# Performance work log

Measured on AMD Instinct MI355X. Metric: run time of the kernel, lower is better.

The kernel has to match this reference:

```python
import jax, jax.numpy as jnp
import numpy as np

N_HEAD = 8
D_HEAD = 128   # dim_k = dim_q = dim_v
SEG_LEN = 512
EPS = 1e-6


def setup_inputs() -> dict:
    key = jax.random.key(0)
    ks = jax.random.split(key, 8)
    B, T, D = 2, 4096, 1024
    scale = 0.02
    x = jax.random.normal(ks[0], (B, T, D), dtype=jnp.float32)
    w_q = jax.random.normal(ks[1], (D, N_HEAD * D_HEAD), dtype=jnp.float32) * scale
    w_k = jax.random.normal(ks[2], (D, N_HEAD * D_HEAD), dtype=jnp.float32) * scale
    w_v = jax.random.normal(ks[3], (D, N_HEAD * D_HEAD), dtype=jnp.float32) * scale
    b_q = jnp.zeros((N_HEAD * D_HEAD,), jnp.float32)
    b_k = jnp.zeros((N_HEAD * D_HEAD,), jnp.float32)
    b_v = jnp.zeros((N_HEAD * D_HEAD,), jnp.float32)
    beta = jnp.zeros((N_HEAD,), jnp.float32)
    return {"x": x, "w_q": w_q, "b_q": b_q, "w_k": w_k, "b_k": b_k,
            "w_v": w_v, "b_v": b_v, "beta": beta}


def _heads(y, B, T):
    # [B,T,H*D] -> [B,H,T,D]
    return y.reshape(B, T, N_HEAD, D_HEAD).transpose(0, 2, 1, 3)


def reference(x, w_q, b_q, w_k, b_k, w_v, b_v, beta):
    B, T, _ = x.shape
    S = T // SEG_LEN
    q = _heads(x @ w_q + b_q, B, T)
    k = _heads(x @ w_k + b_k, B, T)
    v = _heads(x @ w_v + b_v, B, T)

    # segment: [B,H,T,D] -> [S,B,H,L,D]
    def seg(y):
        return y.reshape(B, N_HEAD, S, SEG_LEN, D_HEAD).transpose(2, 0, 1, 3, 4)
    qs, ks_, vs = seg(q), seg(k), seg(v)

    causal = jnp.tril(jnp.ones((SEG_LEN, SEG_LEN), bool))
    gate = jax.nn.sigmoid(beta).reshape(1, N_HEAD, 1, 1)
    inv_sqrt_d = 1.0 / jnp.sqrt(jnp.asarray(D_HEAD, x.dtype))

    def step(carry, segdat):
        M, z = carry                      # M: [B,H,Dk,Dv], z: [B,H,Dk]
        qc, kc, vc = segdat               # [B,H,L,D]
        sq = jax.nn.elu(qc) + 1.0
        sk = jax.nn.elu(kc) + 1.0
        # retrieval from memory BEFORE update
        a_mem = jnp.einsum('bhld,bhde->bhle', sq, M) / (
            jnp.einsum('bhld,bhd->bhl', sq, z)[..., None] + EPS)
        # delta-rule memory update
        retr_k = jnp.einsum('bhld,bhde->bhle', sk, M) / (
            jnp.einsum('bhld,bhd->bhl', sk, z)[..., None] + EPS)
        M = M + jnp.einsum('bhld,bhle->bhde', sk, vc - retr_k)
        z = z + sk.sum(axis=2)
        # local causal dot-product attention within the segment
        scores = jnp.einsum('bhld,bhmd->bhlm', qc, kc) * inv_sqrt_d
        scores = jnp.where(causal, scores, jnp.asarray(-1e30, scores.dtype))
        a_dot = jnp.einsum('bhlm,bhmd->bhld', jax.nn.softmax(scores, axis=-1), vc)
        # long-term context injection
        a = gate * a_mem + (1.0 - gate) * a_dot
        return (M, z), a

    M0 = jnp.zeros((B, N_HEAD, D_HEAD, D_HEAD), x.dtype)
    z0 = jnp.zeros((B, N_HEAD, D_HEAD), x.dtype)
    _, out = jax.lax.scan(step, (M0, z0), (qs, ks_, vs))
    # [S,B,H,L,D] -> [B,T,H*D]
    out = out.transpose(1, 3, 0, 2, 4).reshape(B, T, N_HEAD * D_HEAD)
    # wait: axes of out are [S,B,H,L,D]; reorder to [B,S,L,H,D]
    return out


# fix ordering: define reference properly (overrides above draft path)
def reference(x, w_q, b_q, w_k, b_k, w_v, b_v, beta):
    B, T, _ = x.shape
    S = T // SEG_LEN
    q = _heads(x @ w_q + b_q, B, T)
    k = _heads(x @ w_k + b_k, B, T)
    v = _heads(x @ w_v + b_v, B, T)

    def seg(y):
        return y.reshape(B, N_HEAD, S, SEG_LEN, D_HEAD).transpose(2, 0, 1, 3, 4)
    qs, ks_, vs = seg(q), seg(k), seg(v)

    causal = jnp.tril(jnp.ones((SEG_LEN, SEG_LEN), bool))
    gate = jax.nn.sigmoid(beta).reshape(1, N_HEAD, 1, 1)
    inv_sqrt_d = 1.0 / jnp.sqrt(jnp.asarray(D_HEAD, x.dtype))

    def step(carry, segdat):
        M, z = carry
        qc, kc, vc = segdat
        sq = jax.nn.elu(qc) + 1.0
        sk = jax.nn.elu(kc) + 1.0
        a_mem = jnp.einsum('bhld,bhde->bhle', sq, M) / (
            jnp.einsum('bhld,bhd->bhl', sq, z)[..., None] + EPS)
        retr_k = jnp.einsum('bhld,bhde->bhle', sk, M) / (
            jnp.einsum('bhld,bhd->bhl', sk, z)[..., None] + EPS)
        M = M + jnp.einsum('bhld,bhle->bhde', sk, vc - retr_k)
        z = z + sk.sum(axis=2)
        scores = jnp.einsum('bhld,bhmd->bhlm', qc, kc) * inv_sqrt_d
        scores = jnp.where(causal, scores, jnp.asarray(-1e30, scores.dtype))
        a_dot = jnp.einsum('bhlm,bhmd->bhld', jax.nn.softmax(scores, axis=-1), vc)
        a = gate * a_mem + (1.0 - gate) * a_dot
        return (M, z), a

    M0 = jnp.zeros((B, N_HEAD, D_HEAD, D_HEAD), x.dtype)
    z0 = jnp.zeros((B, N_HEAD, D_HEAD), x.dtype)
    _, out = jax.lax.scan(step, (M0, z0), (qs, ks_, vs))  # [S,B,H,L,D]
    out = out.transpose(1, 0, 3, 2, 4).reshape(B, T, N_HEAD * D_HEAD)
    return out
```

## Files before the change

### kernel.cpp

```cpp
#include <hip/hip_runtime.h>
#include <hip/hip_bf16.h>

typedef __attribute__((ext_vector_type(8))) short bf16x8;
typedef __attribute__((ext_vector_type(4))) float f32x4;
typedef unsigned short u16;
typedef unsigned int u32;

#define DEV static __device__ __forceinline__

DEV float bf2f(u16 u){ u32 x = ((u32)u)<<16; float f; __builtin_memcpy(&f,&x,4); return f; }
DEV u16 f2bf(float f){ u32 x; __builtin_memcpy(&x,&f,4); return (u16)((x + 0x7fffu + ((x>>16)&1u))>>16); }
DEV float elu1(float x){ return x > 0.f ? x + 1.f : __expf(x); }

DEV void gload16(const u16* g, u16* l){
  __builtin_amdgcn_global_load_lds(
      (const __attribute__((address_space(1))) unsigned int*)(g),
      (__attribute__((address_space(3))) unsigned int*)(l), 16, 0, 0);
}

#define MFMA(a,b,c) __builtin_amdgcn_mfma_f32_16x16x32_bf16((a),(b),(c),0,0,0)

#define NB 2
#define NT 4096
#define NH 8
#define DH 128
#define NS 8
#define SL 512
#define ND 1024
#define N3 3072
#define EPS 1e-6f

__global__ __launch_bounds__(256) void k_xc(const float* __restrict__ x, u16* __restrict__ xb){
  int i = blockIdx.x*256 + threadIdx.x;
  const float4 v0 = *(const float4*)(x + (size_t)i*8);
  const float4 v1 = *(const float4*)(x + (size_t)i*8 + 4);
  bf16x8 o;
  o[0]=(short)f2bf(v0.x); o[1]=(short)f2bf(v0.y); o[2]=(short)f2bf(v0.z); o[3]=(short)f2bf(v0.w);
  o[4]=(short)f2bf(v1.x); o[5]=(short)f2bf(v1.y); o[6]=(short)f2bf(v1.z); o[7]=(short)f2bf(v1.w);
  *(bf16x8*)(xb + (size_t)i*8) = o;
}

__global__ __launch_bounds__(256) void k_wt(const float* __restrict__ wq,
                                            const float* __restrict__ wk,
                                            const float* __restrict__ wv,
                                            u16* __restrict__ wt,
                                            float* __restrict__ cs){
  __shared__ float t[32][33];
  const int z = blockIdx.z;
  const float* w = (z==0) ? wq : (z==1 ? wk : wv);
  const int k0 = blockIdx.x*32, n0 = blockIdx.y*32;
  const int tx = threadIdx.x, ty = threadIdx.y;
  if (z==0 && blockIdx.x==0 && blockIdx.y==0){
    const int tid = ty*32 + tx;
#pragma unroll
    for (int i=0;i<64;i++) cs[tid + i*256] = 0.f;
  }
#pragma unroll
  for (int i=0;i<4;i++) t[ty+i*8][tx] = w[(size_t)(k0+ty+i*8)*ND + n0+tx];
  __syncthreads();
#pragma unroll
  for (int i=0;i<4;i++)
    wt[(size_t)(z*ND + n0+ty+i*8)*ND + k0+tx] = f2bf(t[tx][ty+i*8]);
}

__global__ __launch_bounds__(256) void k_gemm(const u16* __restrict__ xb,
                                              const u16* __restrict__ wt,
                                              const float* __restrict__ bq,
                                              const float* __restrict__ bk,
                                              const float* __restrict__ bv,
                                              u16* __restrict__ qkv){
  __shared__ __align__(16) u16 As[128*64];
  __shared__ __align__(16) u16 Bs[128*64];
  const int m0 = blockIdx.x*128, n0 = blockIdx.y*128;
  const int tid = threadIdx.x;
  const int w = tid>>6, lane = tid&63, g = lane>>4, li = lane&15;
  const int wr = w>>1, wc = w&1;
  const int srow = lane>>3;
  const int ssl  = (lane&7) ^ srow;
  f32x4 z4 = {0.f,0.f,0.f,0.f};
  f32x4 acc[4][4];
#pragma unroll
  for (int mi=0;mi<4;mi++)
#pragma unroll
    for (int ni=0;ni<4;ni++) acc[mi][ni] = z4;

  for (int kt=0; kt<16; ++kt){
    const int k0 = kt*64;
#pragma unroll
    for (int i=0;i<4;i++){
      const int c = i*4 + w;
      const int row = c*8 + srow;
      gload16(xb + (size_t)(m0+row)*ND + k0 + ssl*8, As + c*512);
      gload16(wt + (size_t)(n0+row)*ND + k0 + ssl*8, Bs + c*512);
    }
    __syncthreads();
#pragma unroll
    for (int kk=0;kk<2;kk++){
      bf16x8 a[4], bb[4];
#pragma unroll
      for (int mi=0;mi<4;mi++){
        int row = wr*64 + mi*16 + li;
        int slot = kk*4 + g;
        a[mi] = *(const bf16x8*)(As + row*64 + ((slot^(row&7))<<3));
      }
#pragma unroll
      for (int ni=0;ni<4;ni++){
        int row = wc*64 + ni*16 + li;
        int slot = kk*4 + g;
        bb[ni] = *(const bf16x8*)(Bs + row*64 + ((slot^(row&7))<<3));
      }
#pragma unroll
      for (int mi=0;mi<4;mi++)
#pragma unroll
        for (int ni=0;ni<4;ni++)
          acc[mi][ni] = MFMA(a[mi], bb[ni], acc[mi][ni]);
    }
    __syncthreads();
  }
#pragma unroll
  for (int ni=0;ni<4;ni++){
    int n = n0 + wc*64 + ni*16 + li;
    float bias = (n < ND) ? bq[n] : (n < 2*ND ? bk[n-ND] : bv[n-2*ND]);
#pragma unroll
    for (int mi=0;mi<4;mi++)
#pragma unroll
      for (int rr=0;rr<4;rr++){
        int m = m0 + wr*64 + mi*16 + 4*g + rr;
        qkv[(size_t)m*N3 + n] = f2bf(acc[mi][ni][rr] + bias);
      }
  }
}

__global__ __launch_bounds__(256) void k_tr(const u16* __restrict__ qkv,
                                            u16* __restrict__ vt,
                                            u16* __restrict__ pkT,
                                            float* __restrict__ cs){
  __shared__ __align__(4) u16 t[64*66];
  __shared__ float pf[8][64];
  const int t0 = blockIdx.x*64, d0 = blockIdx.y*64;
  const int z = blockIdx.z, bh = z>>1, part = z&1;
  const int b = bh>>3, h = bh&7;
  const int basec = (part ? 2*ND : ND) + h*DH;
  const int tid = threadIdx.x;
  float s0 = 0.f, s1 = 0.f;
#pragma unroll
  for (int i=0;i<8;i++){
    int fp = tid + i*256;
    int row = fp>>5, c2 = (fp&31)*2;
    ushort2 v = *(const ushort2*)(qkv + (size_t)(b*NT + t0+row)*N3 + basec + d0 + c2);
    if (!part){
      float e0 = elu1(bf2f(v.x)), e1 = elu1(bf2f(v.y));
      s0 += e0; s1 += e1;
      v.x = f2bf(e0); v.y = f2bf(e1);
    }
    *(ushort2*)(t + row*66 + c2) = v;
  }
  if (!part){ pf[tid>>5][(tid&31)*2] = s0; pf[tid>>5][(tid&31)*2+1] = s1; }
  __syncthreads();
  u16* dst = part ? vt : pkT;
#pragma unroll
  for (int i=0;i<8;i++){
    int fp = tid + i*256;
    int dr = fp>>5, c2 = (fp&31)*2;
    ushort2 v; v.x = t[c2*66 + dr]; v.y = t[(c2+1)*66 + dr];
    *(ushort2*)(dst + (size_t)(bh*DH + d0+dr)*NT + t0 + c2) = v;
  }
  if (!part && tid < 64){
    float a = 0.f;
#pragma unroll
    for (int r=0;r<8;r++) a += pf[r][tid];
    const int bhs = b*64 + h*8 + (t0>>9);
    atomicAdd(&cs[(size_t)bhs*DH + d0 + tid], a);
  }
}

__global__ __launch_bounds__(512) void k_dinv(const u16* __restrict__ qkv,
                                              const float* __restrict__ cs,
                                              float* __restrict__ dinvK){
  const int bhs = blockIdx.x, half = blockIdx.y;
  const int b = bhs>>6, h = (bhs>>3)&7, s = bhs&7;
  const int tid = threadIdx.x, w = tid>>6, lane = tid&63, grp = lane>>4, li = lane&15;
  __shared__ float zl[128];
  if (tid < 128){
    float a = 0.f;
    for (int sp=0; sp<s; ++sp) a += cs[(size_t)(bhs - s + sp)*DH + tid];
    zl[tid] = a;
  }
  __syncthreads();
#pragma unroll
  for (int it=0; it<8; ++it){
    const int r = half*256 + w*32 + it*4 + grp;
    bf16x8 v = *(const bf16x8*)(qkv + (size_t)(b*NT + s*SL + r)*N3 + ND + h*DH + li*8);
    float p = 0.f;
#pragma unroll
    for (int j=0;j<8;j++) p += elu1(bf2f((u16)v[j])) * zl[li*8+j];
    p += __shfl_xor(p,1); p += __shfl_xor(p,2);
    p += __shfl_xor(p,4); p += __shfl_xor(p,8);
    if (li == 0) dinvK[(size_t)bhs*SL + r] = 1.f/(p + EPS);
  }
}

__global__ __launch_bounds__(512) void k_gram(const u16* __restrict__ pkT,
                                              const u16* __restrict__ vtb,
                                              const float* __restrict__ dinvK,
                                              u16* __restrict__ G, float* __restrict__ Bm){
  const int bhs = blockIdx.x, ec = blockIdx.y;
  const int bh = bhs>>3, s = bhs&7, tb = s*SL;
  const int tid = threadIdx.x, w = tid>>6, lane = tid&63, g = lane>>4, li = lane&15;
  __shared__ __align__(16) u16 Bk[32*512];
  __shared__ __align__(16) u16 Bv[32*512];
  __shared__ float dv[512];
  dv[tid] = dinvK[(size_t)bhs*SL + tid];
#pragma unroll
  for (int i=0;i<4;i++){
    const int ee = i*8 + w;
    const size_t rowo = ((size_t)bh*DH + ec*32 + ee)*NT + tb + ((lane^w)<<3);
    gload16(pkT + rowo, Bk + ee*512);
    gload16(vtb + rowo, Bv + ee*512);
  }
  __syncthreads();
  f32x4 z4 = {0.f,0.f,0.f,0.f};
  f32x4 Ga[2] = {z4,z4}, Ba[2] = {z4,z4};
  const u16* arow = pkT + ((size_t)bh*DH + 16*w + li)*NT + tb;
  for (int ks=0; ks<16; ++ks){
    const int r0 = ks*32 + g*8;
    bf16x8 araw = *(const bf16x8*)(arow + r0);
    float4 d0 = *(const float4*)(dv + r0);
    float4 d1 = *(const float4*)(dv + r0 + 4);
    bf16x8 ascl;
    ascl[0] = (short)f2bf(bf2f((u16)araw[0]) * d0.x);
    ascl[1] = (short)f2bf(bf2f((u16)araw[1]) * d0.y);
    ascl[2] = (short)f2bf(bf2f((u16)araw[2]) * d0.z);
    ascl[3] = (short)f2bf(bf2f((u16)araw[3]) * d0.w);
    ascl[4] = (short)f2bf(bf2f((u16)araw[4]) * d1.x);
    ascl[5] = (short)f2bf(bf2f((u16)araw[5]) * d1.y);
    ascl[6] = (short)f2bf(bf2f((u16)araw[6]) * d1.z);
    ascl[7] = (short)f2bf(bf2f((u16)araw[7]) * d1.w);
    const int slot = ks*4 + g;
#pragma unroll
    for (int ni=0;ni<2;ni++){
      const int ee = ni*16 + li;
      bf16x8 bk8 = *(const bf16x8*)(Bk + ee*512 + ((slot^(li&7))<<3));
      bf16x8 bv8 = *(const bf16x8*)(Bv + ee*512 + ((slot^(li&7))<<3));
      Ga[ni] = MFMA(ascl, bk8, Ga[ni]);
      Ba[ni] = MFMA(araw, bv8, Ba[ni]);
    }
  }
#pragma unroll
  for (int ni=0;ni<2;ni++)
#pragma unroll
    for (int rr=0;rr<4;rr++){
      const int dd = 16*w + 4*g + rr;
      const int ee = ec*32 + ni*16 + li;
      G[((size_t)bhs*DH + dd)*DH + ee] = f2bf(Ga[ni][rr]);
      Bm[((size_t)bhs*DH + dd)*DH + ee] = Ba[ni][rr];
    }
}

__global__ __launch_bounds__(512) void k_scan(const u16* __restrict__ G,
                                              const float* __restrict__ Bm,
                                              u16* __restrict__ MTs){
  const int bh = blockIdx.x;
  const int tid = threadIdx.x, w = tid>>6, lane = tid&63, g = lane>>4, li = lane&15;
  __shared__ __align__(16) u16 MT[16384];
  for (int i = tid; i < 16384; i += 512) MT[i] = 0;
  __syncthreads();
  for (int s=0;s<NS;s++){
    const size_t bhs = (size_t)bh*NS + s;
    for (int f = tid; f < 2048; f += 512){
      int e = f>>4, sl = f&15;
      bf16x8 v = *(const bf16x8*)(MT + e*128 + ((sl^(e&7))<<3));
      *(bf16x8*)(MTs + bhs*16384 + e*128 + sl*8) = v;
    }
    __syncthreads();
    f32x4 z4 = {0.f,0.f,0.f,0.f};
    f32x4 acc[8];
#pragma unroll
    for (int i=0;i<8;i++) acc[i] = z4;
#pragma unroll
    for (int ks=0;ks<4;ks++){
      bf16x8 a = *(const bf16x8*)(G + (bhs*DH + 16*w + li)*DH + ks*32 + g*8);
#pragma unroll
      for (int ni=0;ni<8;ni++){
        int e = ni*16 + li;
        int sl = ks*4 + g;
        bf16x8 bfr = *(const bf16x8*)(MT + e*128 + ((sl^(e&7))<<3));
        acc[ni] = MFMA(a, bfr, acc[ni]);
      }
    }
    __syncthreads();
#pragma unroll
    for (int ni=0;ni<8;ni++)
#pragma unroll
      for (int rr=0;rr<4;rr++){
        int dd = 16*w + 4*g + rr, ee = ni*16 + li;
        float delta = Bm[(bhs*DH + dd)*DH + ee] - acc[ni][rr];
        int idx = ee*128 + (((dd>>3)^(ee&7))<<3) + (dd&7);
        MT[idx] = f2bf(bf2f(MT[idx]) + delta);
      }
    __syncthreads();
  }
}

__global__ __launch_bounds__(512) void k_attn(const u16* __restrict__ qkv,
                                              const u16* __restrict__ vtb,
                                              const u16* __restrict__ MTs,
                                              const float* __restrict__ cs,
                                              const float* __restrict__ beta,
                                              float* __restrict__ out){
  const int bhs = blockIdx.x, half = blockIdx.y;
  const int b = bhs>>6, h = (bhs>>3)&7, s = bhs&7, bh = bhs>>3;
  const int tid = threadIdx.x, w = tid>>6, lane = tid&63, g = lane>>4, li = lane&15;
  const int jq = (w < 4) ? (half + 2*w) : (15 - half - 2*(w-4));
  const int qb = jq*32;
  const float gate = 1.f/(1.f + __expf(-beta[h]));
  const float isd = 0.08838834764831845f;
  const float L2E = 1.4426950408889634f;
  __shared__ __align__(16) u16 P[8*1024];
  __shared__ float zl[128];
  __shared__ float dinvW[8][32];
  u16* Pw = P + w*1024;

  if (tid < 128){
    float a = 0.f;
    for (int sp=0; sp<s; ++sp) a += cs[(size_t)(bhs - s + sp)*DH + tid];
    zl[tid] = a;
  }
  __syncthreads();

  {
    const int r = qb + (lane&31);
    const int dh = (lane>>5)*64;
    const u16* qrow = qkv + (size_t)(b*NT + s*SL + r)*N3 + h*DH + dh;
    float p = 0.f;
#pragma unroll
    for (int j=0;j<64;j+=8){
      bf16x8 v = *(const bf16x8*)(qrow + j);
#pragma unroll
      for (int t=0;t<8;t++) p += elu1(bf2f((u16)v[t])) * zl[dh + j + t];
    }
    p += __shfl_xor(p, 32);
    if (lane < 32) dinvW[w][lane] = 1.f/(p + EPS);
  }

  bf16x8 qf[2][4];
#pragma unroll
  for (int mf=0; mf<2; ++mf)
#pragma unroll
    for (int kf=0; kf<4; ++kf)
      qf[mf][kf] = *(const bf16x8*)(qkv + (size_t)(b*NT + s*SL + qb + mf*16 + li)*N3 + h*DH + kf*32 + g*8);

  f32x4 z4 = {0.f,0.f,0.f,0.f};
  f32x4 O[2][8];
  float lr[2][4];
#pragma unroll
  for (int mf=0;mf<2;++mf){
#pragma unroll
    for (int nf=0;nf<8;++nf) O[mf][nf] = z4;
#pragma unroll
    for (int rr=0;rr<4;++rr) lr[mf][rr] = 0.f;
  }

  const int nch = jq + 1;
  for (int c=0; c<nch; ++c){
    const int kb = c*32;
    f32x4 sa[2][2];
#pragma unroll
    for (int mf=0;mf<2;++mf)
#pragma unroll
      for (int nf=0;nf<2;++nf) sa[mf][nf] = z4;
#pragma unroll
    for (int kf=0; kf<4; ++kf)
#pragma unroll
      for (int nf=0; nf<2; ++nf){
        bf16x8 bk8 = *(const bf16x8*)(qkv + (size_t)(b*NT + s*SL + kb + nf*16 + li)*N3 + ND + h*DH + kf*32 + g*8);
        sa[0][nf] = MFMA(qf[0][kf], bk8, sa[0][nf]);
        sa[1][nf] = MFMA(qf[1][kf], bk8, sa[1][nf]);
      }
    float pv[2][2][4];
#pragma unroll
    for (int mf=0;mf<2;++mf)
#pragma unroll
      for (int rr=0;rr<4;++rr){
        int row = qb + mf*16 + 4*g + rr;
        float rs = 0.f;
#pragma unroll
        for (int nf=0;nf<2;++nf){
          int col = kb + nf*16 + li;
          float sc = sa[mf][nf][rr]*isd;
          float p = (col > row) ? 0.f : exp2f(sc*L2E);
          pv[mf][nf][rr] = p; rs += p;
        }
        rs += __shfl_xor(rs, 1); rs += __shfl_xor(rs, 2);
        rs += __shfl_xor(rs, 4); rs += __shfl_xor(rs, 8);
        lr[mf][rr] += rs;
      }
#pragma unroll
    for (int mf=0;mf<2;++mf)
#pragma unroll
      for (int nf=0;nf<2;++nf)
#pragma unroll
        for (int rr=0;rr<4;++rr){
          int row = mf*16 + 4*g + rr, col = nf*16 + li;
          Pw[row*32 + (((col>>3)^(row&3))<<3) + (col&7)] = f2bf(pv[mf][nf][rr]);
        }
    bf16x8 pa[2];
#pragma unroll
    for (int mf=0;mf<2;++mf){
      int row = mf*16 + li;
      pa[mf] = *(const bf16x8*)(Pw + row*32 + ((g^(row&3))<<3));
    }
#pragma unroll
    for (int nf=0;nf<8;++nf){
      bf16x8 bv8 = *(const bf16x8*)(vtb + ((size_t)bh*DH + nf*16 + li)*NT + s*SL + kb + g*8);
      O[0][nf] = MFMA(pa[0], bv8, O[0][nf]);
      O[1][nf] = MFMA(pa[1], bv8, O[1][nf]);
    }
  }

  f32x4 Am[2][8];
#pragma unroll
  for (int mf=0;mf<2;++mf)
#pragma unroll
    for (int nf=0;nf<8;++nf) Am[mf][nf] = z4;
#pragma unroll
  for (int ks=0;ks<4;++ks){
    bf16x8 pq[2];
#pragma unroll
    for (int mf=0;mf<2;++mf){
      bf16x8 raw = qf[mf][ks];
#pragma unroll
      for (int j=0;j<8;j++) raw[j] = (short)f2bf(elu1(bf2f((u16)raw[j])));
      pq[mf] = raw;
    }
#pragma unroll
    for (int nf=0;nf<8;++nf){
      bf16x8 bfr = *(const bf16x8*)(MTs + ((size_t)bhs*DH + nf*16 + li)*DH + ks*32 + g*8);
      Am[0][nf] = MFMA(pq[0], bfr, Am[0][nf]);
      Am[1][nf] = MFMA(pq[1], bfr, Am[1][nf]);
    }
  }

  const float og = 1.f - gate;
#pragma unroll
  for (int mf=0;mf<2;++mf)
#pragma unroll
    for (int rr=0;rr<4;++rr){
      int row = qb + mf*16 + 4*g + rr;
      float invd = og / lr[mf][rr];
      float dv = gate * dinvW[w][row - qb];
#pragma unroll
      for (int nf=0;nf<8;++nf)
        out[(size_t)(b*NT + s*SL + row)*ND + h*DH + nf*16 + li] =
            O[mf][nf][rr]*invd + Am[mf][nf][rr]*dv;
    }
}

extern "C" void kernel_launch(void* const* d_in, const int* in_sizes, int n_in,
                              void* d_out, int out_size, void* d_ws, size_t ws_size,
                              hipStream_t stream) {
  (void)in_sizes; (void)n_in; (void)out_size; (void)ws_size;
  const float* x    = (const float*)d_in[0];
  const float* wq   = (const float*)d_in[1];
  const float* bq   = (const float*)d_in[2];
  const float* wk   = (const float*)d_in[3];
  const float* bk   = (const float*)d_in[4];
  const float* wv   = (const float*)d_in[5];
  const float* bv   = (const float*)d_in[6];
  const float* beta = (const float*)d_in[7];
  float* out = (float*)d_out;
  char* ws = (char*)d_ws;

  u16*   wt  = (u16*)  (ws + 0);
  u16*   qkv = (u16*)  (ws + 6291456);
  u16*   vt  = (u16*)  (ws + 56623104);
  u16*   pkT = (u16*)  (ws + 73400320);
  u16*   G   = (u16*)  (ws + 90177536);
  float* Bm  = (float*)(ws + 94371840);
  u16*   MTs = (u16*)  (ws + 102760448);
  float* cs  = (float*)(ws + 106954752);
  u16*   xb  = vt;
  float* dinvK = (float*)(ws + 107020288);

  hipLaunchKernelGGL(k_xc,    dim3(4096),    dim3(256),  0, stream, x, xb);
  hipLaunchKernelGGL(k_wt,    dim3(32,32,3), dim3(32,8), 0, stream, wq, wk, wv, wt, cs);
  hipLaunchKernelGGL(k_gemm,  dim3(64,24),   dim3(256),  0, stream, xb, wt, bq, bk, bv, qkv);
  hipLaunchKernelGGL(k_tr,    dim3(64,2,32), dim3(256),  0, stream, qkv, vt, pkT, cs);
  hipLaunchKernelGGL(k_dinv,  dim3(128,2),   dim3(512),  0, stream, qkv, cs, dinvK);
  hipLaunchKernelGGL(k_gram,  dim3(128,4),   dim3(512),  0, stream, pkT, vt, dinvK, G, Bm);
  hipLaunchKernelGGL(k_scan,  dim3(16),      dim3(512),  0, stream, G, Bm, MTs);
  hipLaunchKernelGGL(k_attn,  dim3(128,2),   dim3(512),  0, stream, qkv, vt, MTs, cs, beta, out);
}
```

Baseline: 201.6 us.

## Split memory scan across column blocks and stage GEMM epilogue through LDS

```diff
diff --git a/kernel.cpp b/kernel.cpp
--- a/kernel.cpp
+++ b/kernel.cpp
@@ -117,17 +117,28 @@
     }
     __syncthreads();
   }
+
+  u16* SC = (w < 2 ? As : Bs) + (w&1)*4096;
 #pragma unroll
   for (int ni=0;ni<4;ni++){
-    int n = n0 + wc*64 + ni*16 + li;
-    float bias = (n < ND) ? bq[n] : (n < 2*ND ? bk[n-ND] : bv[n-2*ND]);
+    const int n = n0 + wc*64 + ni*16 + li;
+    const float bias = (n < ND) ? bq[n] : (n < 2*ND ? bk[n-ND] : bv[n-2*ND]);
 #pragma unroll
     for (int mi=0;mi<4;mi++)
 #pragma unroll
       for (int rr=0;rr<4;rr++){
-        int m = m0 + wr*64 + mi*16 + 4*g + rr;
-        qkv[(size_t)m*N3 + n] = f2bf(acc[mi][ni][rr] + bias);
+        const int ml = mi*16 + 4*g + rr;
+        const int nl = ni*16 + li;
+        SC[ml*64 + (((nl>>3)^(ml&7))<<3) + (nl&7)] = f2bf(acc[mi][ni][rr] + bias);
       }
+  }
+  __syncthreads();
+  const int rb = lane>>3, cb = lane&7;
+#pragma unroll
+  for (int j=0;j<8;j++){
+    const int r = j*8 + rb;
+    bf16x8 v = *(const bf16x8*)(SC + r*64 + ((cb^(r&7))<<3));
+    *(bf16x8*)(qkv + (size_t)(m0 + wr*64 + r)*N3 + n0 + wc*64 + cb*8) = v;
   }
 }
 
@@ -260,44 +271,39 @@
 __global__ __launch_bounds__(512) void k_scan(const u16* __restrict__ G,
                                               const float* __restrict__ Bm,
                                               u16* __restrict__ MTs){
-  const int bh = blockIdx.x;
+  const int bh = blockIdx.x, ec = blockIdx.y;
   const int tid = threadIdx.x, w = tid>>6, lane = tid&63, g = lane>>4, li = lane&15;
-  __shared__ __align__(16) u16 MT[16384];
-  for (int i = tid; i < 16384; i += 512) MT[i] = 0;
-  __syncthreads();
+  __shared__ float MF[16*132];
+  __shared__ __align__(16) u16 MB[16*128];
+  for (int i = tid; i < 16*132; i += 512) MF[i] = 0.f;
+  __syncthreads();
+  const int dr = w*16 + li;
   for (int s=0;s<NS;s++){
     const size_t bhs = (size_t)bh*NS + s;
-    for (int f = tid; f < 2048; f += 512){
-      int e = f>>4, sl = f&15;
-      bf16x8 v = *(const bf16x8*)(MT + e*128 + ((sl^(e&7))<<3));
-      *(bf16x8*)(MTs + bhs*16384 + e*128 + sl*8) = v;
+    if (tid < 256){
+      const int e = tid>>4, dg = tid&15;
+      const float* src = MF + e*132 + dg*8;
+      bf16x8 v;
+#pragma unroll
+      for (int j=0;j<8;j++) v[j] = (short)f2bf(src[j]);
+      *(bf16x8*)(MTs + bhs*16384 + (size_t)(ec*16+e)*128 + dg*8) = v;
+      *(bf16x8*)(MB + e*128 + ((dg^(e&7))<<3)) = v;
     }
     __syncthreads();
-    f32x4 z4 = {0.f,0.f,0.f,0.f};
-    f32x4 acc[8];
-#pragma unroll
-    for (int i=0;i<8;i++) acc[i] = z4;
+    f32x4 acc = {0.f,0.f,0.f,0.f};
 #pragma unroll
     for (int ks=0;ks<4;ks++){
-      bf16x8 a = *(const bf16x8*)(G + (bhs*DH + 16*w + li)*DH + ks*32 + g*8);
-#pragma unroll
-      for (int ni=0;ni<8;ni++){
-        int e = ni*16 + li;
-        int sl = ks*4 + g;
-        bf16x8 bfr = *(const bf16x8*)(MT + e*128 + ((sl^(e&7))<<3));
-        acc[ni] = MFMA(a, bfr, acc[ni]);
-      }
-    }
-    __syncthreads();
-#pragma unroll
-    for (int ni=0;ni<8;ni++)
-#pragma unroll
-      for (int rr=0;rr<4;rr++){
-        int dd = 16*w + 4*g + rr, ee = ni*16 + li;
-        float delta = Bm[(bhs*DH + dd)*DH + ee] - acc[ni][rr];
-        int idx = ee*128 + (((dd>>3)^(ee&7))<<3) + (dd&7);
-        MT[idx] = f2bf(bf2f(MT[idx]) + delta);
-      }
+      bf16x8 a = *(const bf16x8*)(G + ((size_t)bhs*DH + dr)*DH + ks*32 + g*8);
+      const int sl = ks*4 + g;
+      bf16x8 bfr = *(const bf16x8*)(MB + li*128 + ((sl^(li&7))<<3));
+      acc = MFMA(a, bfr, acc);
+    }
+#pragma unroll
+    for (int rr=0;rr<4;rr++){
+      const int d = w*16 + 4*g + rr;
+      const float delta = Bm[((size_t)bhs*DH + d)*DH + ec*16 + li] - acc[rr];
+      MF[li*132 + d] += delta;
+    }
     __syncthreads();
   }
 }
@@ -488,6 +494,6 @@
   hipLaunchKernelGGL(k_tr,    dim3(64,2,32), dim3(256),  0, stream, qkv, vt, pkT, cs);
   hipLaunchKernelGGL(k_dinv,  dim3(128,2),   dim3(512),  0, stream, qkv, cs, dinvK);
   hipLaunchKernelGGL(k_gram,  dim3(128,4),   dim3(512),  0, stream, pkT, vt, dinvK, G, Bm);
-  hipLaunchKernelGGL(k_scan,  dim3(16),      dim3(512),  0, stream, G, Bm, MTs);
+  hipLaunchKernelGGL(k_scan,  dim3(16,8),    dim3(512),  0, stream, G, Bm, MTs);
   hipLaunchKernelGGL(k_attn,  dim3(128,2),   dim3(512),  0, stream, qkv, vt, MTs, cs, beta, out);
 }
```

Result: faster. 186.5 us (-7.5%).
